# Optimization experiments

Hardware: AMD Instinct MI355X
Metric: run time of the kernel (lower is better)

The kernel has to match this reference:

```python
import jax, jax.numpy as jnp
import numpy as np

EPS = 1e-5

def _ln(x, g, b):
    mu = x.mean(-1, keepdims=True)
    var = ((x - mu) ** 2).mean(-1, keepdims=True)
    return (x - mu) / jnp.sqrt(var + EPS) * g + b

def setup_inputs() -> dict:
    key = jax.random.key(0)
    ks = jax.random.split(key, 24)
    B, S, I, H, D, F = 64, 512, 32, 64, 128, 256
    def w(k, shape, fan_in):
        return jax.random.uniform(k, shape, jnp.float32, -1.0, 1.0) / np.sqrt(fan_in)
    return {
        'x': jax.random.normal(ks[0], (B, S, I), jnp.float32),
        'W_ih': w(ks[1], (H, I), H), 'b_ih': w(ks[2], (H,), H),
        'W_hh': w(ks[3], (H, H), H), 'b_hh': w(ks[4], (H,), H),
        'Wp': w(ks[5], (D, H), H), 'bp': w(ks[6], (D,), H),
        'Wqkv': w(ks[7], (3 * D, D), D), 'bqkv': jnp.zeros((3 * D,), jnp.float32),
        'Wo': w(ks[8], (D, D), D), 'bo': jnp.zeros((D,), jnp.float32),
        'g1': jnp.ones((D,), jnp.float32), 'be1': jnp.zeros((D,), jnp.float32),
        'W1': w(ks[9], (F, D), D), 'b1': w(ks[10], (F,), D),
        'W2': w(ks[11], (D, F), F), 'b2': w(ks[12], (D,), F),
        'g2': jnp.ones((D,), jnp.float32), 'be2': jnp.zeros((D,), jnp.float32),
        'gn': jnp.ones((D,), jnp.float32), 'bn': jnp.zeros((D,), jnp.float32),
        'Wf': w(ks[13], (I, D), D), 'bf': w(ks[14], (I,), D),
    }

def reference(x, W_ih, b_ih, W_hh, b_hh, Wp, bp, Wqkv, bqkv, Wo, bo,
              g1, be1, W1, b1, W2, b2, g2, be2, gn, bn, Wf, bf):
    B, S, I = x.shape
    H = W_ih.shape[0]
    D = Wp.shape[0]
    nh = 8
    hd = D // nh

    # RNNCell tanh recurrence over time (sequential, vectorized over batch)
    xs = jnp.swapaxes(x, 0, 1)  # (S, B, I)
    def step(h, x_t):
        h = jnp.tanh(x_t @ W_ih.T + b_ih + h @ W_hh.T + b_hh)
        return h, h
    _, hs = jax.lax.scan(step, jnp.zeros((B, H), x.dtype), xs)  # (S, B, H)

    proj = hs @ Wp.T + bp  # (S, B, D)

    # TransformerEncoderLayer (post-norm, relu), dropout = identity (eval)
    qkv = proj @ Wqkv.T + bqkv  # (S, B, 3D)
    q, k, v = jnp.split(qkv, 3, axis=-1)
    q = q.reshape(S, B, nh, hd)
    k = k.reshape(S, B, nh, hd)
    v = v.reshape(S, B, nh, hd)
    scores = jnp.einsum('sbhd,tbhd->bhst', q, k) / np.sqrt(hd)
    attn = jax.nn.softmax(scores, axis=-1)
    ctx = jnp.einsum('bhst,tbhd->sbhd', attn, v).reshape(S, B, D)
    attn_out = ctx @ Wo.T + bo
    x1 = _ln(proj + attn_out, g1, be1)
    ff = jax.nn.relu(x1 @ W1.T + b1) @ W2.T + b2
    x2 = _ln(x1 + ff, g2, be2)

    out = _ln(x2 + proj, gn, bn)
    pooled = out.mean(axis=0)  # (B, D)
    return jnp.tanh(pooled @ Wf.T + bf)
```

## Files before the change

### kernel.cpp

```cpp
#include <hip/hip_runtime.h>
#include <hip/hip_bf16.h>

#define BB 64
#define SS 512
#define II 32
#define HH 64
#define DD 128
#define FF 256
#define NHEAD 8
#define HDIM 16
#define NTOK (SS*BB)

typedef short bf16x8 __attribute__((ext_vector_type(8)));
typedef float f32x4  __attribute__((ext_vector_type(4)));

__device__ __forceinline__ float fast_tanh(float x) {
    float ax = fabsf(x);
    float e = __expf(-2.0f * ax);
    float r = (1.0f - e) * __builtin_amdgcn_rcpf(1.0f + e);
    return copysignf(r, x);
}

__device__ __forceinline__ float bcast(float v, int lane) {
    return __int_as_float(__builtin_amdgcn_readlane(__float_as_int(v), lane));
}

__device__ __forceinline__ short f2bf(float x) {
    unsigned u = __float_as_uint(x);
    return (short)((u + 0x7FFFu + ((u >> 16) & 1u)) >> 16);
}

__global__ __launch_bounds__(256) void k_xw(const float* __restrict__ x,
                                            const float* __restrict__ W_ih,
                                            const float* __restrict__ b_ih,
                                            const float* __restrict__ b_hh,
                                            float* __restrict__ xw) {
    int idx = blockIdx.x * 256 + threadIdx.x;
    int j  = idx & (HH - 1);
    int sb = idx >> 6;
    int s  = sb >> 6;
    int b  = sb & (BB - 1);
    const float* xr = x + (b * SS + s) * II;
    const float* wr = W_ih + j * II;
    float acc = b_ih[j] + b_hh[j];
    #pragma unroll
    for (int k = 0; k < II; k += 4) {
        float4 xv = *(const float4*)(xr + k);
        float4 wv = *(const float4*)(wr + k);
        acc += xv.x * wv.x + xv.y * wv.y + xv.z * wv.z + xv.w * wv.w;
    }
    xw[idx] = acc;
}

__global__ __launch_bounds__(64, 1) void k_rnn(const float* __restrict__ xw,
                                               const float* __restrict__ W_hh,
                                               float* __restrict__ hs) {
    int b = blockIdx.x;
    int j = threadIdx.x;
    float w[HH];
    #pragma unroll
    for (int k = 0; k < HH; k++) w[k] = W_hh[j * HH + k];

    float hv = 0.0f;
    float xv0 = xw[(0 * BB + b) * HH + j];
    float xv1 = xw[(1 * BB + b) * HH + j];
    for (int t = 0; t < SS; t++) {
        int tn = (t < SS - 2) ? t + 2 : t;
        float xnext = xw[(tn * BB + b) * HH + j];
        float a0 = xv0, a1 = 0.f, a2 = 0.f, a3 = 0.f;
        #pragma unroll
        for (int k = 0; k < HH; k += 4) {
            a0 = fmaf(w[k + 0], bcast(hv, k + 0), a0);
            a1 = fmaf(w[k + 1], bcast(hv, k + 1), a1);
            a2 = fmaf(w[k + 2], bcast(hv, k + 2), a2);
            a3 = fmaf(w[k + 3], bcast(hv, k + 3), a3);
        }
        hv = fast_tanh((a0 + a1) + (a2 + a3));
        hs[(t * BB + b) * HH + j] = hv;
        xv0 = xv1;
        xv1 = xnext;
    }
}

template<int K, bool RELU>
__global__ __launch_bounds__(256) void k_gemm_w128(const float* __restrict__ A,
                                                   const float* __restrict__ W,
                                                   const float* __restrict__ bias,
                                                   float* __restrict__ C, int N) {
    __shared__ short As[128 * 40];
    __shared__ short Ws[128 * 40];
    int tid = threadIdx.x;
    int wid = tid >> 6, lane = tid & 63;
    int col = lane & 15, quad = lane >> 4;
    int rowBase = blockIdx.x * 128, colBase = blockIdx.y * 128;

    f32x4 acc[2][8];
    #pragma unroll
    for (int nt = 0; nt < 8; nt++) {
        float bv = bias[colBase + nt * 16 + col];
        #pragma unroll
        for (int mt = 0; mt < 2; mt++) {
            acc[mt][nt][0] = bv; acc[mt][nt][1] = bv;
            acc[mt][nt][2] = bv; acc[mt][nt][3] = bv;
        }
    }

    int arow = tid >> 1, akb = (tid & 1) * 16;

    for (int kb = 0; kb < K; kb += 32) {
        {
            const float4* ap = (const float4*)(A + (size_t)(rowBase + arow) * K + kb + akb);
            float4 v0 = ap[0], v1 = ap[1], v2 = ap[2], v3 = ap[3];
            short t0[8], t1[8];
            t0[0]=f2bf(v0.x); t0[1]=f2bf(v0.y); t0[2]=f2bf(v0.z); t0[3]=f2bf(v0.w);
            t0[4]=f2bf(v1.x); t0[5]=f2bf(v1.y); t0[6]=f2bf(v1.z); t0[7]=f2bf(v1.w);
            t1[0]=f2bf(v2.x); t1[1]=f2bf(v2.y); t1[2]=f2bf(v2.z); t1[3]=f2bf(v2.w);
            t1[4]=f2bf(v3.x); t1[5]=f2bf(v3.y); t1[6]=f2bf(v3.z); t1[7]=f2bf(v3.w);
            *(int4*)&As[arow * 40 + akb]     = *(int4*)t0;
            *(int4*)&As[arow * 40 + akb + 8] = *(int4*)t1;
        }
        {
            const float4* wp = (const float4*)(W + (size_t)(colBase + arow) * K + kb + akb);
            float4 v0 = wp[0], v1 = wp[1], v2 = wp[2], v3 = wp[3];
            short t0[8], t1[8];
            t0[0]=f2bf(v0.x); t0[1]=f2bf(v0.y); t0[2]=f2bf(v0.z); t0[3]=f2bf(v0.w);
            t0[4]=f2bf(v1.x); t0[5]=f2bf(v1.y); t0[6]=f2bf(v1.z); t0[7]=f2bf(v1.w);
            t1[0]=f2bf(v2.x); t1[1]=f2bf(v2.y); t1[2]=f2bf(v2.z); t1[3]=f2bf(v2.w);
            t1[4]=f2bf(v3.x); t1[5]=f2bf(v3.y); t1[6]=f2bf(v3.z); t1[7]=f2bf(v3.w);
            *(int4*)&Ws[arow * 40 + akb]     = *(int4*)t0;
            *(int4*)&Ws[arow * 40 + akb + 8] = *(int4*)t1;
        }
        __syncthreads();

        bf16x8 af[2], wf[8];
        #pragma unroll
        for (int mt = 0; mt < 2; mt++)
            af[mt] = *(const bf16x8*)&As[(wid * 32 + mt * 16 + col) * 40 + quad * 8];
        #pragma unroll
        for (int nt = 0; nt < 8; nt++)
            wf[nt] = *(const bf16x8*)&Ws[(nt * 16 + col) * 40 + quad * 8];
        #pragma unroll
        for (int mt = 0; mt < 2; mt++)
            #pragma unroll
            for (int nt = 0; nt < 8; nt++)
                acc[mt][nt] = __builtin_amdgcn_mfma_f32_16x16x32_bf16(af[mt], wf[nt], acc[mt][nt], 0, 0, 0);
        __syncthreads();
    }

    #pragma unroll
    for (int mt = 0; mt < 2; mt++) {
        #pragma unroll
        for (int r = 0; r < 4; r++) {
            int m = rowBase + wid * 32 + mt * 16 + quad * 4 + r;
            float* crow = C + (size_t)m * N + colBase;
            #pragma unroll
            for (int nt = 0; nt < 8; nt++) {
                float v = acc[mt][nt][r];
                if (RELU) v = fmaxf(v, 0.f);
                crow[nt * 16 + col] = v;
            }
        }
    }
}

template<int K, int NLN>
__global__ __launch_bounds__(256) void k_gemm_ln(const float* __restrict__ A,
                                                 const float* __restrict__ W,
                                                 const float* __restrict__ bias,
                                                 const float* __restrict__ res1,
                                                 const float* __restrict__ g1v,
                                                 const float* __restrict__ be1v,
                                                 const float* __restrict__ res2,
                                                 const float* __restrict__ g2v,
                                                 const float* __restrict__ be2v,
                                                 float* __restrict__ out) {
    __shared__ short As[128 * 40];
    __shared__ short Ws[128 * 40];
    int tid = threadIdx.x;
    int wid = tid >> 6, lane = tid & 63;
    int col = lane & 15, quad = lane >> 4;
    int rowBase = blockIdx.x * 128;

    f32x4 acc[2][8];
    #pragma unroll
    for (int nt = 0; nt < 8; nt++) {
        float bv = bias[nt * 16 + col];
        #pragma unroll
        for (int mt = 0; mt < 2; mt++) {
            acc[mt][nt][0] = bv; acc[mt][nt][1] = bv;
            acc[mt][nt][2] = bv; acc[mt][nt][3] = bv;
        }
    }

    int arow = tid >> 1, akb = (tid & 1) * 16;

    for (int kb = 0; kb < K; kb += 32) {
        {
            const float4* ap = (const float4*)(A + (size_t)(rowBase + arow) * K + kb + akb);
            float4 v0 = ap[0], v1 = ap[1], v2 = ap[2], v3 = ap[3];
            short t0[8], t1[8];
            t0[0]=f2bf(v0.x); t0[1]=f2bf(v0.y); t0[2]=f2bf(v0.z); t0[3]=f2bf(v0.w);
            t0[4]=f2bf(v1.x); t0[5]=f2bf(v1.y); t0[6]=f2bf(v1.z); t0[7]=f2bf(v1.w);
            t1[0]=f2bf(v2.x); t1[1]=f2bf(v2.y); t1[2]=f2bf(v2.z); t1[3]=f2bf(v2.w);
            t1[4]=f2bf(v3.x); t1[5]=f2bf(v3.y); t1[6]=f2bf(v3.z); t1[7]=f2bf(v3.w);
            *(int4*)&As[arow * 40 + akb]     = *(int4*)t0;
            *(int4*)&As[arow * 40 + akb + 8] = *(int4*)t1;
        }
        {
            const float4* wp = (const float4*)(W + (size_t)arow * K + kb + akb);
            float4 v0 = wp[0], v1 = wp[1], v2 = wp[2], v3 = wp[3];
            short t0[8], t1[8];
            t0[0]=f2bf(v0.x); t0[1]=f2bf(v0.y); t0[2]=f2bf(v0.z); t0[3]=f2bf(v0.w);
            t0[4]=f2bf(v1.x); t0[5]=f2bf(v1.y); t0[6]=f2bf(v1.z); t0[7]=f2bf(v1.w);
            t1[0]=f2bf(v2.x); t1[1]=f2bf(v2.y); t1[2]=f2bf(v2.z); t1[3]=f2bf(v2.w);
            t1[4]=f2bf(v3.x); t1[5]=f2bf(v3.y); t1[6]=f2bf(v3.z); t1[7]=f2bf(v3.w);
            *(int4*)&Ws[arow * 40 + akb]     = *(int4*)t0;
            *(int4*)&Ws[arow * 40 + akb + 8] = *(int4*)t1;
        }
        __syncthreads();

        bf16x8 af[2], wf[8];
        #pragma unroll
        for (int mt = 0; mt < 2; mt++)
            af[mt] = *(const bf16x8*)&As[(wid * 32 + mt * 16 + col) * 40 + quad * 8];
        #pragma unroll
        for (int nt = 0; nt < 8; nt++)
            wf[nt] = *(const bf16x8*)&Ws[(nt * 16 + col) * 40 + quad * 8];
        #pragma unroll
        for (int mt = 0; mt < 2; mt++)
            #pragma unroll
            for (int nt = 0; nt < 8; nt++)
                acc[mt][nt] = __builtin_amdgcn_mfma_f32_16x16x32_bf16(af[mt], wf[nt], acc[mt][nt], 0, 0, 0);
        __syncthreads();
    }

    float ga[8], ba[8], gb[8], bb[8];
    #pragma unroll
    for (int nt = 0; nt < 8; nt++) {
        ga[nt] = g1v[nt * 16 + col]; ba[nt] = be1v[nt * 16 + col];
        if (NLN == 2) { gb[nt] = g2v[nt * 16 + col]; bb[nt] = be2v[nt * 16 + col]; }
    }

    #pragma unroll
    for (int mt = 0; mt < 2; mt++) {
        #pragma unroll
        for (int r = 0; r < 4; r++) {
            int m = rowBase + wid * 32 + mt * 16 + quad * 4 + r;
            const float* rr1 = res1 + (size_t)m * DD;
            float v[8];
            float s = 0.f;
            #pragma unroll
            for (int nt = 0; nt < 8; nt++) {
                v[nt] = acc[mt][nt][r] + rr1[nt * 16 + col];
                s += v[nt];
            }
            #pragma unroll
            for (int off = 1; off < 16; off <<= 1) s += __shfl_xor(s, off, 64);
            float mu = s * (1.0f / 128.0f);
            float vs = 0.f;
            #pragma unroll
            for (int nt = 0; nt < 8; nt++) { v[nt] -= mu; vs += v[nt] * v[nt]; }
            #pragma unroll
            for (int off = 1; off < 16; off <<= 1) vs += __shfl_xor(vs, off, 64);
            float rstd = rsqrtf(vs * (1.0f / 128.0f) + 1e-5f);
            #pragma unroll
            for (int nt = 0; nt < 8; nt++) v[nt] = v[nt] * rstd * ga[nt] + ba[nt];

            if (NLN == 2) {
                const float* rr2 = res2 + (size_t)m * DD;
                float s2 = 0.f;
                #pragma unroll
                for (int nt = 0; nt < 8; nt++) {
                    v[nt] += rr2[nt * 16 + col];
                    s2 += v[nt];
                }
                #pragma unroll
                for (int off = 1; off < 16; off <<= 1) s2 += __shfl_xor(s2, off, 64);
                float mu2 = s2 * (1.0f / 128.0f);
                float vs2 = 0.f;
                #pragma unroll
                for (int nt = 0; nt < 8; nt++) { v[nt] -= mu2; vs2 += v[nt] * v[nt]; }
                #pragma unroll
                for (int off = 1; off < 16; off <<= 1) vs2 += __shfl_xor(vs2, off, 64);
                float rstd2 = rsqrtf(vs2 * (1.0f / 128.0f) + 1e-5f);
                #pragma unroll
                for (int nt = 0; nt < 8; nt++) v[nt] = v[nt] * rstd2 * gb[nt] + bb[nt];
            }

            float* orow = out + (size_t)m * DD;
            #pragma unroll
            for (int nt = 0; nt < 8; nt++) orow[nt * 16 + col] = v[nt];
        }
    }
}

__global__ __launch_bounds__(256, 2) void k_attn(const float* __restrict__ qkv,
                                                 float* __restrict__ ctx) {
    int bh = blockIdx.x;
    int b = bh >> 3, h = bh & 7;
    __shared__ short Vt[HDIM][SS];
    __shared__ short Pb[4][2][16 * 64];
    int tid = threadIdx.x;

    for (int t = tid; t < SS; t += 256) {
        const float* base = qkv + (size_t)(t * BB + b) * 384 + h * 16;
        float4 v0 = *(const float4*)(base + 256);
        float4 v1 = *(const float4*)(base + 260);
        float4 v2 = *(const float4*)(base + 264);
        float4 v3 = *(const float4*)(base + 268);
        int u = t & 63;
        int pos = (t & ~63) | (((u & 15) << 2) | (u >> 4));
        Vt[0][pos]=f2bf(v0.x);  Vt[1][pos]=f2bf(v0.y);  Vt[2][pos]=f2bf(v0.z);  Vt[3][pos]=f2bf(v0.w);
        Vt[4][pos]=f2bf(v1.x);  Vt[5][pos]=f2bf(v1.y);  Vt[6][pos]=f2bf(v1.z);  Vt[7][pos]=f2bf(v1.w);
        Vt[8][pos]=f2bf(v2.x);  Vt[9][pos]=f2bf(v2.y);  Vt[10][pos]=f2bf(v2.z); Vt[11][pos]=f2bf(v2.w);
        Vt[12][pos]=f2bf(v3.x); Vt[13][pos]=f2bf(v3.y); Vt[14][pos]=f2bf(v3.z); Vt[15][pos]=f2bf(v3.w);
    }
    __syncthreads();

    int wid = tid >> 6, lane = tid & 63;
    int col = lane & 15, quad = lane >> 4;
    const float qscale = 0.25f * 1.44269504f;

    bf16x8 kf[32];
    #pragma unroll
    for (int kt = 0; kt < 32; kt++) {
        bf16x8 f = (bf16x8)(short)0;
        if (quad < 2) {
            const float* ksrc = qkv + (size_t)((kt * 16 + col) * BB + b) * 384 + 128 + h * 16 + quad * 8;
            float4 ka = *(const float4*)ksrc;
            float4 kb2 = *(const float4*)(ksrc + 4);
            f[0]=f2bf(ka.x);  f[1]=f2bf(ka.y);  f[2]=f2bf(ka.z);  f[3]=f2bf(ka.w);
            f[4]=f2bf(kb2.x); f[5]=f2bf(kb2.y); f[6]=f2bf(kb2.z); f[7]=f2bf(kb2.w);
        }
        kf[kt] = f;
    }

    for (int sub = 0; sub < 8; sub++) {
        int q0 = wid * 128 + sub * 16;

        bf16x8 qf = (bf16x8)(short)0;
        if (quad < 2) {
            const float* qsrc = qkv + (size_t)((q0 + col) * BB + b) * 384 + h * 16 + quad * 8;
            float4 qa = *(const float4*)qsrc;
            float4 qb = *(const float4*)(qsrc + 4);
            qf[0]=f2bf(qa.x*qscale); qf[1]=f2bf(qa.y*qscale);
            qf[2]=f2bf(qa.z*qscale); qf[3]=f2bf(qa.w*qscale);
            qf[4]=f2bf(qb.x*qscale); qf[5]=f2bf(qb.y*qscale);
            qf[6]=f2bf(qb.z*qscale); qf[7]=f2bf(qb.w*qscale);
        }

        float l0 = 0.f, l1 = 0.f, l2 = 0.f, l3 = 0.f;
        f32x4 O = {0.f, 0.f, 0.f, 0.f};
        #pragma unroll
        for (int c = 0; c < 8; c++) {
            short* pbuf = &Pb[wid][c & 1][0];
            float p[4][4];
            #pragma unroll
            for (int kk = 0; kk < 4; kk++) {
                f32x4 z = {0.f, 0.f, 0.f, 0.f};
                f32x4 S = __builtin_amdgcn_mfma_f32_16x16x32_bf16(qf, kf[c * 4 + kk], z, 0, 0, 0);
                p[kk][0] = exp2f(S[0]); p[kk][1] = exp2f(S[1]);
                p[kk][2] = exp2f(S[2]); p[kk][3] = exp2f(S[3]);
                l0 += p[kk][0]; l1 += p[kk][1]; l2 += p[kk][2]; l3 += p[kk][3];
            }
            #pragma unroll
            for (int r = 0; r < 4; r++) {
                unsigned w0 = (unsigned)(unsigned short)f2bf(p[0][r])
                            | ((unsigned)(unsigned short)f2bf(p[1][r]) << 16);
                unsigned w1 = (unsigned)(unsigned short)f2bf(p[2][r])
                            | ((unsigned)(unsigned short)f2bf(p[3][r]) << 16);
                *(uint2*)&pbuf[(4 * quad + r) * 64 + col * 4] = make_uint2(w0, w1);
            }
            #pragma unroll
            for (int half = 0; half < 2; half++) {
                int tb = c * 64 + half * 32;
                bf16x8 pf = *(const bf16x8*)&pbuf[col * 64 + half * 32 + quad * 8];
                bf16x8 vf = *(const bf16x8*)&Vt[col][tb + quad * 8];
                O = __builtin_amdgcn_mfma_f32_16x16x32_bf16(pf, vf, O, 0, 0, 0);
            }
        }

        float l[4] = {l0, l1, l2, l3};
        #pragma unroll
        for (int r = 0; r < 4; r++) {
            #pragma unroll
            for (int off = 1; off < 16; off <<= 1) l[r] += __shfl_xor(l[r], off, 64);
            float inv = __builtin_amdgcn_rcpf(l[r]);
            int q = q0 + 4 * quad + r;
            ctx[(size_t)(q * BB + b) * DD + h * 16 + col] = O[r] * inv;
        }
    }
}

__global__ __launch_bounds__(256) void k_poolfinal(const float* __restrict__ outln,
                                                   const float* __restrict__ Wf,
                                                   const float* __restrict__ bfv,
                                                   float* __restrict__ out) {
    int b = blockIdx.x;
    int tid = threadIdx.x;
    __shared__ float part[256];
    __shared__ float pooled[128];
    int d = tid & 127, half = tid >> 7;
    float s = 0.f;
    int s0 = half * 256;
    #pragma unroll 8
    for (int si = s0; si < s0 + 256; si++)
        s += outln[(size_t)(si * BB + b) * DD + d];
    part[tid] = s;
    __syncthreads();
    if (tid < 128) pooled[tid] = (part[tid] + part[tid + 128]) * (1.0f / SS);
    __syncthreads();
    if (tid < 32) {
        const float* wr = Wf + tid * DD;
        float acc = bfv[tid];
        #pragma unroll
        for (int k = 0; k < DD; k += 4) {
            float4 wv = *(const float4*)(wr + k);
            acc += pooled[k] * wv.x + pooled[k + 1] * wv.y
                 + pooled[k + 2] * wv.z + pooled[k + 3] * wv.w;
        }
        out[b * 32 + tid] = fast_tanh(acc);
    }
}

extern "C" void kernel_launch(void* const* d_in, const int* in_sizes, int n_in,
                              void* d_out, int out_size, void* d_ws, size_t ws_size,
                              hipStream_t stream) {
    const float* x    = (const float*)d_in[0];
    const float* W_ih = (const float*)d_in[1];
    const float* b_ih = (const float*)d_in[2];
    const float* W_hh = (const float*)d_in[3];
    const float* b_hh = (const float*)d_in[4];
    const float* Wp   = (const float*)d_in[5];
    const float* bp   = (const float*)d_in[6];
    const float* Wqkv = (const float*)d_in[7];
    const float* bqkv = (const float*)d_in[8];
    const float* Wo   = (const float*)d_in[9];
    const float* bo   = (const float*)d_in[10];
    const float* g1   = (const float*)d_in[11];
    const float* be1  = (const float*)d_in[12];
    const float* W1   = (const float*)d_in[13];
    const float* b1   = (const float*)d_in[14];
    const float* W2   = (const float*)d_in[15];
    const float* b2   = (const float*)d_in[16];
    const float* g2   = (const float*)d_in[17];
    const float* be2  = (const float*)d_in[18];
    const float* gn   = (const float*)d_in[19];
    const float* bn   = (const float*)d_in[20];
    const float* Wf   = (const float*)d_in[21];
    const float* bf   = (const float*)d_in[22];
    float* out = (float*)d_out;
    float* ws  = (float*)d_ws;

    float* proj   = ws + 0;
    float* qkv    = ws + 4194304;
    float* outln  = ws + 4194304;
    float* xw     = ws + 16777216;
    float* hsbuf  = ws + 18874368;
    float* ctx    = ws + 16777216;
    float* x1     = ws + 20971520;
    float* ff1    = ws + 25165824;

    k_xw<<<8192, 256, 0, stream>>>(x, W_ih, b_ih, b_hh, xw);
    k_rnn<<<64, 64, 0, stream>>>(xw, W_hh, hsbuf);
    k_gemm_w128<64,  false><<<dim3(256, 1), 256, 0, stream>>>(hsbuf, Wp, bp, proj, 128);
    k_gemm_w128<128, false><<<dim3(256, 3), 256, 0, stream>>>(proj, Wqkv, bqkv, qkv, 384);
    k_attn<<<512, 256, 0, stream>>>(qkv, ctx);
    k_gemm_ln<128, 1><<<256, 256, 0, stream>>>(ctx, Wo, bo, proj, g1, be1,
                                               nullptr, nullptr, nullptr, x1);
    k_gemm_w128<128, true ><<<dim3(256, 2), 256, 0, stream>>>(x1, W1, b1, ff1, 256);
    k_gemm_ln<256, 2><<<256, 256, 0, stream>>>(ff1, W2, b2, x1, g2, be2,
                                               proj, gn, bn, outln);
    k_poolfinal<<<64, 256, 0, stream>>>(outln, Wf, bf, out);
}
```

Baseline: 420.1 us.

## Fuse post-RNN transformer stages into one persistent kernel with grid barriers

Merges the projection, QKV GEMM, attention, output projection with layernorm, FFN GEMMs and pooling into a single persistent 256-block kernel. Stages are separated by atomic-counter grid barriers, and shared memory is reused across stages. The aim is to remove per-kernel launch gaps and tail effects. In exchange it relies on all blocks being co-resident, serialises the attention over two passes per block, and adds barrier spin overhead.

```diff
diff --git a/kernel.cpp b/kernel.cpp
--- a/kernel.cpp
+++ b/kernel.cpp
@@ -28,6 +28,17 @@
 __device__ __forceinline__ short f2bf(float x) {
     unsigned u = __float_as_uint(x);
     return (short)((u + 0x7FFFu + ((u >> 16) & 1u)) >> 16);
+}
+
+__device__ __forceinline__ void gbar(unsigned* c, unsigned nblk) {
+    __syncthreads();
+    if (threadIdx.x == 0) {
+        __hip_atomic_fetch_add(c, 1u, __ATOMIC_ACQ_REL, __HIP_MEMORY_SCOPE_AGENT);
+        while (__hip_atomic_load(c, __ATOMIC_ACQUIRE, __HIP_MEMORY_SCOPE_AGENT) < nblk)
+            __builtin_amdgcn_s_sleep(2);
+        __threadfence();
+    }
+    __syncthreads();
 }
 
 __global__ __launch_bounds__(256) void k_xw(const float* __restrict__ x,
@@ -82,17 +93,19 @@
     }
 }
 
+
 template<int K, bool RELU>
-__global__ __launch_bounds__(256) void k_gemm_w128(const float* __restrict__ A,
-                                                   const float* __restrict__ W,
-                                                   const float* __restrict__ bias,
-                                                   float* __restrict__ C, int N) {
-    __shared__ short As[128 * 40];
-    __shared__ short Ws[128 * 40];
+__device__ __forceinline__ void gemm_tile(char* smem,
+                                          const float* __restrict__ A,
+                                          const float* __restrict__ W,
+                                          const float* __restrict__ bias,
+                                          float* __restrict__ C, int N,
+                                          int rowBase, int colBase) {
+    short* As = (short*)smem;
+    short* Ws = (short*)(smem + 10240);
     int tid = threadIdx.x;
     int wid = tid >> 6, lane = tid & 63;
     int col = lane & 15, quad = lane >> 4;
-    int rowBase = blockIdx.x * 128, colBase = blockIdx.y * 128;
 
     f32x4 acc[2][8];
     #pragma unroll
@@ -164,22 +177,22 @@
 }
 
 template<int K, int NLN>
-__global__ __launch_bounds__(256) void k_gemm_ln(const float* __restrict__ A,
-                                                 const float* __restrict__ W,
-                                                 const float* __restrict__ bias,
-                                                 const float* __restrict__ res1,
-                                                 const float* __restrict__ g1v,
-                                                 const float* __restrict__ be1v,
-                                                 const float* __restrict__ res2,
-                                                 const float* __restrict__ g2v,
-                                                 const float* __restrict__ be2v,
-                                                 float* __restrict__ out) {
-    __shared__ short As[128 * 40];
-    __shared__ short Ws[128 * 40];
+__device__ __forceinline__ void gemm_ln_tile(char* smem,
+                                             const float* __restrict__ A,
+                                             const float* __restrict__ W,
+                                             const float* __restrict__ bias,
+                                             const float* __restrict__ res1,
+                                             const float* __restrict__ g1v,
+                                             const float* __restrict__ be1v,
+                                             const float* __restrict__ res2,
+                                             const float* __restrict__ g2v,
+                                             const float* __restrict__ be2v,
+                                             float* __restrict__ out, int rowBase) {
+    short* As = (short*)smem;
+    short* Ws = (short*)(smem + 10240);
     int tid = threadIdx.x;
     int wid = tid >> 6, lane = tid & 63;
     int col = lane & 15, quad = lane >> 4;
-    int rowBase = blockIdx.x * 128;
 
     f32x4 acc[2][8];
     #pragma unroll
@@ -294,12 +307,11 @@
     }
 }
 
-__global__ __launch_bounds__(256, 2) void k_attn(const float* __restrict__ qkv,
-                                                 float* __restrict__ ctx) {
-    int bh = blockIdx.x;
+__device__ __forceinline__ void attn_one(char* smem, const float* __restrict__ qkv,
+                                         float* __restrict__ ctx, int bh) {
     int b = bh >> 3, h = bh & 7;
-    __shared__ short Vt[HDIM][SS];
-    __shared__ short Pb[4][2][16 * 64];
+    short (*Vt)[SS] = (short(*)[SS])smem;
+    short* PbBase = (short*)(smem + 16384);
     int tid = threadIdx.x;
 
     for (int t = tid; t < SS; t += 256) {
@@ -353,7 +365,7 @@
         f32x4 O = {0.f, 0.f, 0.f, 0.f};
         #pragma unroll
         for (int c = 0; c < 8; c++) {
-            short* pbuf = &Pb[wid][c & 1][0];
+            short* pbuf = PbBase + (wid * 2 + (c & 1)) * 1024;
             float p[4][4];
             #pragma unroll
             for (int kk = 0; kk < 4; kk++) {
@@ -392,14 +404,14 @@
     }
 }
 
-__global__ __launch_bounds__(256) void k_poolfinal(const float* __restrict__ outln,
-                                                   const float* __restrict__ Wf,
-                                                   const float* __restrict__ bfv,
-                                                   float* __restrict__ out) {
-    int b = blockIdx.x;
+__device__ __forceinline__ void poolfinal_one(char* smem,
+                                              const float* __restrict__ outln,
+                                              const float* __restrict__ Wf,
+                                              const float* __restrict__ bfv,
+                                              float* __restrict__ out, int b) {
+    float* part = (float*)smem;
+    float* pooled = (float*)(smem + 1024);
     int tid = threadIdx.x;
-    __shared__ float part[256];
-    __shared__ float pooled[128];
     int d = tid & 127, half = tid >> 7;
     float s = 0.f;
     int s0 = half * 256;
@@ -421,6 +433,54 @@
         }
         out[b * 32 + tid] = fast_tanh(acc);
     }
+}
+
+__global__ __launch_bounds__(256) void k_mega(
+        const float* __restrict__ hsbuf,
+        const float* __restrict__ Wp,   const float* __restrict__ bp,
+        const float* __restrict__ Wqkv, const float* __restrict__ bqkv,
+        const float* __restrict__ Wo,   const float* __restrict__ bo,
+        const float* __restrict__ g1,   const float* __restrict__ be1,
+        const float* __restrict__ W1,   const float* __restrict__ b1,
+        const float* __restrict__ W2,   const float* __restrict__ b2,
+        const float* __restrict__ g2,   const float* __restrict__ be2,
+        const float* __restrict__ gn,   const float* __restrict__ bn,
+        const float* __restrict__ Wf,   const float* __restrict__ bf,
+        float* __restrict__ proj, float* __restrict__ qkv,
+        float* __restrict__ ctx,  float* __restrict__ x1,
+        float* __restrict__ ff1,  float* __restrict__ outln,
+        float* __restrict__ out,  unsigned* __restrict__ ctr) {
+    __shared__ __align__(16) char smem[32768];
+    int bid = blockIdx.x;
+
+    gemm_tile<64, false>(smem, hsbuf, Wp, bp, proj, 128, bid * 128, 0);
+    gbar(&ctr[0], 256);
+
+    for (int t = bid; t < 768; t += 256)
+        gemm_tile<128, false>(smem, proj, Wqkv, bqkv, qkv, 384,
+                              (t & 255) * 128, (t >> 8) * 128);
+    gbar(&ctr[1], 256);
+
+    for (int bh = bid; bh < 512; bh += 256) {
+        attn_one(smem, qkv, ctx, bh);
+        __syncthreads();
+    }
+    gbar(&ctr[2], 256);
+
+    gemm_ln_tile<128, 1>(smem, ctx, Wo, bo, proj, g1, be1,
+                         nullptr, nullptr, nullptr, x1, bid * 128);
+    gbar(&ctr[3], 256);
+
+    for (int t = bid; t < 512; t += 256)
+        gemm_tile<128, true>(smem, x1, W1, b1, ff1, 256,
+                             (t & 255) * 128, (t >> 8) * 128);
+    gbar(&ctr[4], 256);
+
+    gemm_ln_tile<256, 2>(smem, ff1, W2, b2, x1, g2, be2,
+                         proj, gn, bn, outln, bid * 128);
+    gbar(&ctr[5], 256);
+
+    if (bid < 64) poolfinal_one(smem, outln, Wf, bf, out, bid);
 }
 
 extern "C" void kernel_launch(void* const* d_in, const int* in_sizes, int n_in,
@@ -460,16 +520,13 @@
     float* ctx    = ws + 16777216;
     float* x1     = ws + 20971520;
     float* ff1    = ws + 25165824;
-
+    unsigned* ctr = (unsigned*)(ws + 33554432);
+
+    hipMemsetAsync(ctr, 0, 64, stream);
     k_xw<<<8192, 256, 0, stream>>>(x, W_ih, b_ih, b_hh, xw);
     k_rnn<<<64, 64, 0, stream>>>(xw, W_hh, hsbuf);
-    k_gemm_w128<64,  false><<<dim3(256, 1), 256, 0, stream>>>(hsbuf, Wp, bp, proj, 128);
-    k_gemm_w128<128, false><<<dim3(256, 3), 256, 0, stream>>>(proj, Wqkv, bqkv, qkv, 384);
-    k_attn<<<512, 256, 0, stream>>>(qkv, ctx);
-    k_gemm_ln<128, 1><<<256, 256, 0, stream>>>(ctx, Wo, bo, proj, g1, be1,
-                                               nullptr, nullptr, nullptr, x1);
-    k_gemm_w128<128, true ><<<dim3(256, 2), 256, 0, stream>>>(x1, W1, b1, ff1, 256);
-    k_gemm_ln<256, 2><<<256, 256, 0, stream>>>(ff1, W2, b2, x1, g2, be2,
-                                               proj, gn, bn, outln);
-    k_poolfinal<<<64, 256, 0, stream>>>(outln, Wf, bf, out);
-}
+    k_mega<<<256, 256, 0, stream>>>(hsbuf, Wp, bp, Wqkv, bqkv, Wo, bo,
+                                    g1, be1, W1, b1, W2, b2, g2, be2,
+                                    gn, bn, Wf, bf,
+                                    proj, qkv, ctx, x1, ff1, outln, out, ctr);
+}
```

After: 638.5 us. 52.0% more time.
